# Kernel tuning notes

Hardware: AMD Instinct MI355X
Metric: run time of the kernel (lower is better)

## Reference

```python
import jax, jax.numpy as jnp
import numpy as np

B, L, H, HEADS = 4, 2048, 512, 8
D = H // HEADS  # 64


def setup_inputs() -> dict:
    key = jax.random.key(0)
    ks = jax.random.split(key, 13)
    s = 0.02
    return {
        "q_in": jax.random.normal(ks[0], (B, L, H), jnp.float32),
        "k_in": jax.random.normal(ks[1], (B, L, H), jnp.float32),
        "v_in": jax.random.normal(ks[2], (B, L, H), jnp.float32),
        "Wq_w": jax.random.normal(ks[3], (H, H), jnp.float32) * s,
        "Wq_b": jax.random.normal(ks[4], (H,), jnp.float32) * s,
        "Wk_w": jax.random.normal(ks[5], (H, H), jnp.float32) * s,
        "Wk_b": jax.random.normal(ks[6], (H,), jnp.float32) * s,
        "Wv_w": jax.random.normal(ks[7], (H, H), jnp.float32) * s,
        "Wv_b": jax.random.normal(ks[8], (H,), jnp.float32) * s,
        "Wo_w": jax.random.normal(ks[9], (H, H), jnp.float32) * s,
        "Wo_b": jax.random.normal(ks[10], (H,), jnp.float32) * s,
        "Wp_w": jax.random.normal(ks[11], (2 * L - 1, D), jnp.float32) * s,
        "Wp_b": jax.random.normal(ks[12], (2 * L - 1,), jnp.float32) * s,
    }


def _skew(p):
    # p: (b, h, l, 2l-1) -> relative-position bias (b, h, l, l) via pad/flatten/reshape skew trick
    b, h, l, _ = p.shape
    p = jnp.pad(p, ((0, 0), (0, 0), (0, 0), (0, 1)))          # (b,h,l,2l)
    p = p.reshape(b, h, 2 * l * l)
    p = jnp.pad(p, ((0, 0), (0, 0), (0, l - 1)))               # (b,h,(l+1)(2l-1))
    p = p.reshape(b, h, l + 1, 2 * l - 1)
    return p[:, :, :-1, -l:]                                   # (b,h,l,l)


def reference(q_in, k_in, v_in, Wq_w, Wq_b, Wk_w, Wk_b, Wv_w, Wv_b, Wo_w, Wo_b, Wp_w, Wp_b):
    b, l, hid = q_in.shape
    q = q_in @ Wq_w.T + Wq_b
    k = k_in @ Wk_w.T + Wk_b
    v = v_in @ Wv_w.T + Wv_b
    # (b, l, h*d) -> (b, h, l, d)
    to_heads = lambda x: x.reshape(b, l, HEADS, D).transpose(0, 2, 1, 3)
    q, k, v = to_heads(q), to_heads(k), to_heads(v)
    q = q / jnp.sqrt(jnp.asarray(D, q.dtype))  # scaling applied BEFORE posenc, as in original
    scores = jnp.einsum('bhid,bhjd->bhij', q, k)
    pos = _skew(q @ Wp_w.T + Wp_b)             # posenc linear applied to scaled q
    scores = scores + pos
    attn = jax.nn.softmax(scores, axis=-1)     # (b,h,l,l)
    # Original torch.einsum('b h l l, b h l d -> b h l d') takes the DIAGONAL of attn
    diag = jnp.diagonal(attn, axis1=-2, axis2=-1)  # (b,h,l)
    out = diag[..., None] * v                       # (b,h,l,d)
    out = out.transpose(0, 2, 1, 3).reshape(b, l, hid)
    return out @ Wo_w.T + Wo_b
```

## Files before the change

### kernel.cpp

```cpp
#include <hip/hip_runtime.h>
#include <cstdint>


typedef unsigned short u16;
typedef __bf16 bf16x8 __attribute__((ext_vector_type(8)));
typedef __bf16 bf16x2 __attribute__((ext_vector_type(2)));
typedef float  f32x16 __attribute__((ext_vector_type(16)));
typedef uint32_t __attribute__((address_space(1))) as1_u32;
typedef uint32_t __attribute__((address_space(3))) as3_u32;

__device__ __forceinline__ u16 f2bf(float f) {
  __bf16 h = (__bf16)f;
  return __builtin_bit_cast(u16, h);
}
__device__ __forceinline__ uint32_t pkbf(float a, float b) {
  bf16x2 v; v[0] = (__bf16)a; v[1] = (__bf16)b;
  return __builtin_bit_cast(uint32_t, v);
}
__device__ __forceinline__ float bf2f(u16 u) {
  return __uint_as_float(((uint32_t)u) << 16);
}
__device__ __forceinline__ void gl_lds16(const void* g, void* l) {
  __builtin_amdgcn_global_load_lds((const as1_u32*)g, (as3_u32*)l, 16, 0, 0);
}

__global__ __launch_bounds__(256) void prep_kernel(
    const float* __restrict__ qin, const float* __restrict__ kin, const float* __restrict__ vin,
    const float* __restrict__ wq,  const float* __restrict__ wk,  const float* __restrict__ wv,
    const float* __restrict__ wo,  const float* __restrict__ wp,
    u16* __restrict__ xq, u16* __restrict__ xk, u16* __restrict__ xv,
    u16* __restrict__ bwq, u16* __restrict__ bwk, u16* __restrict__ bwv,
    u16* __restrict__ bwo, u16* __restrict__ bwp) {
  long u = (long)blockIdx.x * 256 + threadIdx.x;
  const float* src; u16* dst; long off; float qs = 1.0f;
  if      (u < 524288L)  { src = qin; dst = xq;  off = u; }
  else if (u < 1048576L) { src = kin; dst = xk;  off = u - 524288L; }
  else if (u < 1572864L) { src = vin; dst = xv;  off = u - 1048576L; }
  else if (u < 1605632L) { src = wq;  dst = bwq; off = u - 1572864L; qs = 0.18033688f; }
  else if (u < 1638400L) { src = wk;  dst = bwk; off = u - 1605632L; }
  else if (u < 1671168L) { src = wv;  dst = bwv; off = u - 1638400L; }
  else if (u < 1703936L) { src = wo;  dst = bwo; off = u - 1671168L; }
  else if (u < 1736696L) { src = wp;  dst = bwp; off = u - 1703936L; }
  else {
    long o = (u - 1736696L) * 8 + 262080L;
    uint4 z = {0u, 0u, 0u, 0u};
    *(uint4*)(bwp + o) = z;
    return;
  }
  const float4* s4 = (const float4*)(src + off * 8);
  float4 a = s4[0], b = s4[1];
  uint32_t p0 = pkbf(a.x * qs, a.y * qs);
  uint32_t p1 = pkbf(a.z * qs, a.w * qs);
  uint32_t p2 = pkbf(b.x * qs, b.y * qs);
  uint32_t p3 = pkbf(b.z * qs, b.w * qs);
  uint4 o = {p0, p1, p2, p3};
  *(uint4*)(dst + off * 8) = o;
}

__global__ __launch_bounds__(256) void gemm_bt(
    const u16* __restrict__ A, const u16* __restrict__ W, const float* __restrict__ bias,
    float* __restrict__ ofp) {
  __shared__ u16 Al[128 * 32];
  __shared__ u16 Bl[128 * 32];
  const int tid = threadIdx.x;
  const int lane = tid & 63, w = tid >> 6;
  const int wi = w >> 1, wj = w & 1;
  const int m0 = (blockIdx.x >> 2) * 128, n0 = (blockIdx.x & 3) * 128;
  const int l31 = lane & 31;

  float bv0 = bias[n0 + 64 * wj + l31];
  float bv1 = bias[n0 + 64 * wj + 32 + l31];
  f32x16 acc[2][2];
#pragma unroll
  for (int i = 0; i < 2; ++i)
#pragma unroll
    for (int r = 0; r < 16; ++r) { acc[i][0][r] = bv0; acc[i][1][r] = bv1; }

  for (int kb = 0; kb < 16; ++kb) {
#pragma unroll
    for (int c = 0; c < 2; ++c) {
      int s = c * 256 + w * 64 + lane;
      int r = s >> 2, ch = s & 3;
      int gch = ch ^ ((r >> 1) & 3);
      gl_lds16(A + (long)(m0 + r) * 512 + kb * 32 + gch * 8, (char*)Al + (c * 256 + w * 64) * 16);
      gl_lds16(W + (long)(n0 + r) * 512 + kb * 32 + gch * 8, (char*)Bl + (c * 256 + w * 64) * 16);
    }
    __syncthreads();
    bf16x8 af[2][2], bfr[2][2];
#pragma unroll
    for (int mt = 0; mt < 2; ++mt)
#pragma unroll
      for (int ks = 0; ks < 2; ++ks) {
        int r = 64 * wi + 32 * mt + l31;
        int ch = 2 * ks + (lane >> 5);
        af[mt][ks] = *(const bf16x8*)((char*)Al + (r * 4 + (ch ^ ((r >> 1) & 3))) * 16);
      }
#pragma unroll
    for (int nt = 0; nt < 2; ++nt)
#pragma unroll
      for (int ks = 0; ks < 2; ++ks) {
        int r = 64 * wj + 32 * nt + l31;
        int ch = 2 * ks + (lane >> 5);
        bfr[nt][ks] = *(const bf16x8*)((char*)Bl + (r * 4 + (ch ^ ((r >> 1) & 3))) * 16);
      }
#pragma unroll
    for (int mt = 0; mt < 2; ++mt)
#pragma unroll
      for (int nt = 0; nt < 2; ++nt)
#pragma unroll
        for (int ks = 0; ks < 2; ++ks)
          acc[mt][nt] = __builtin_amdgcn_mfma_f32_32x32x16_bf16(af[mt][ks], bfr[nt][ks],
                                                                acc[mt][nt], 0, 0, 0);
    __syncthreads();
  }
#pragma unroll
  for (int nt = 0; nt < 2; ++nt) {
    int n = n0 + 64 * wj + 32 * nt + l31;
#pragma unroll
    for (int mt = 0; mt < 2; ++mt) {
#pragma unroll
      for (int r = 0; r < 16; ++r) {
        int row = m0 + 64 * wi + 32 * mt + (r & 3) + 8 * (r >> 2) + 4 * (lane >> 5);
        ofp[(long)row * 512 + n] = acc[mt][nt][r];
      }
    }
  }
}

__global__ __launch_bounds__(256) void qkv_gemm(
    const u16* __restrict__ xq, const u16* __restrict__ xk, const u16* __restrict__ xv,
    const u16* __restrict__ wqp, const u16* __restrict__ wkp, const u16* __restrict__ wvp,
    const float* __restrict__ bq, const float* __restrict__ bk, const float* __restrict__ bv,
    u16* __restrict__ oq, u16* __restrict__ ok, u16* __restrict__ ov) {
  __shared__ u16 Al[128 * 32];
  __shared__ u16 Bl[128 * 32];
  const int mat = blockIdx.x >> 8;
  const int tile = blockIdx.x & 255;
  const u16* A = (mat == 0) ? xq : (mat == 1) ? xk : xv;
  const u16* W = (mat == 0) ? wqp : (mat == 1) ? wkp : wvp;
  const float* bias = (mat == 0) ? bq : (mat == 1) ? bk : bv;
  u16* obf = (mat == 0) ? oq : (mat == 1) ? ok : ov;
  const float bsc = (mat == 0) ? 0.18033688f : 1.0f;

  const int tid = threadIdx.x;
  const int lane = tid & 63, w = tid >> 6;
  const int wi = w >> 1, wj = w & 1;
  const int m0 = (tile >> 2) * 128, n0 = (tile & 3) * 128;
  const int l31 = lane & 31;

  float bv0 = bias[n0 + 64 * wj + l31] * bsc;
  float bv1 = bias[n0 + 64 * wj + 32 + l31] * bsc;
  f32x16 acc[2][2];
#pragma unroll
  for (int i = 0; i < 2; ++i)
#pragma unroll
    for (int r = 0; r < 16; ++r) { acc[i][0][r] = bv0; acc[i][1][r] = bv1; }

  for (int kb = 0; kb < 16; ++kb) {
#pragma unroll
    for (int c = 0; c < 2; ++c) {
      int s = c * 256 + w * 64 + lane;
      int r = s >> 2, ch = s & 3;
      int gch = ch ^ ((r >> 1) & 3);
      gl_lds16(A + (long)(m0 + r) * 512 + kb * 32 + gch * 8, (char*)Al + (c * 256 + w * 64) * 16);
      gl_lds16(W + (long)(n0 + r) * 512 + kb * 32 + gch * 8, (char*)Bl + (c * 256 + w * 64) * 16);
    }
    __syncthreads();
    bf16x8 af[2][2], bfr[2][2];
#pragma unroll
    for (int mt = 0; mt < 2; ++mt)
#pragma unroll
      for (int ks = 0; ks < 2; ++ks) {
        int r = 64 * wi + 32 * mt + l31;
        int ch = 2 * ks + (lane >> 5);
        af[mt][ks] = *(const bf16x8*)((char*)Al + (r * 4 + (ch ^ ((r >> 1) & 3))) * 16);
      }
#pragma unroll
    for (int nt = 0; nt < 2; ++nt)
#pragma unroll
      for (int ks = 0; ks < 2; ++ks) {
        int r = 64 * wj + 32 * nt + l31;
        int ch = 2 * ks + (lane >> 5);
        bfr[nt][ks] = *(const bf16x8*)((char*)Bl + (r * 4 + (ch ^ ((r >> 1) & 3))) * 16);
      }
#pragma unroll
    for (int mt = 0; mt < 2; ++mt)
#pragma unroll
      for (int nt = 0; nt < 2; ++nt)
#pragma unroll
        for (int ks = 0; ks < 2; ++ks)
          acc[mt][nt] = __builtin_amdgcn_mfma_f32_32x32x16_bf16(af[mt][ks], bfr[nt][ks],
                                                                acc[mt][nt], 0, 0, 0);
    __syncthreads();
  }
#pragma unroll
  for (int nt = 0; nt < 2; ++nt) {
    int n = n0 + 64 * wj + 32 * nt + l31;
#pragma unroll
    for (int mt = 0; mt < 2; ++mt) {
#pragma unroll
      for (int r = 0; r < 16; ++r) {
        int row = m0 + 64 * wi + 32 * mt + (r & 3) + 8 * (r >> 2) + 4 * (lane >> 5);
        int b = row >> 11, l = row & 2047, h = n >> 6, d = n & 63;
        obf[(((long)(b * 8 + h)) * 2048 + l) * 64 + d] = f2bf(acc[mt][nt][r]);
      }
    }
  }
}

__global__ __launch_bounds__(256, 4) void attn_kernel(
    const u16* __restrict__ qw, const u16* __restrict__ kw, const u16* __restrict__ vw,
    const u16* __restrict__ wpw, const float* __restrict__ wpb, u16* __restrict__ outp) {
  __shared__ u16 Pl[283 * 66];
  __shared__ float sdiag[64];
  __shared__ float rssum[128];
  __shared__ float attw[64];

  const int tid = threadIdx.x, lane = tid & 63, w = tid >> 6;
  const int wi = w >> 1, wj = w & 1;
  const int sbi = blockIdx.x;
  const int kk_ = sbi >> 3;
  const int bh = (sbi & 7) + 8 * (kk_ >> 5);
  const int it = kk_ & 31;
  const int i0 = it * 64, base = 1984 - i0;
  const u16* qb = qw + (long)bh * 2048 * 64;
  const u16* kb = kw + (long)bh * 2048 * 64;
  const u16* vb = vw + (long)bh * 2048 * 64;

  const int l31 = lane & 31, lh = lane >> 5;
  const int iibase = 32 * wi + 4 * lh;

  bf16x8 aq[4];
  {
    int row = i0 + 32 * wi + l31;
    const u16* p = qb + (long)row * 64 + lh * 8;
#pragma unroll
    for (int kk = 0; kk < 4; ++kk) aq[kk] = *(const bf16x8*)(p + kk * 16);
  }

  float rsum[16];
#pragma unroll
  for (int r = 0; r < 16; ++r) rsum[r] = 0.f;

  auto pblock = [&](int g) {
    int brow = base + 64 * g + 32 * wj + l31;
    const u16* bp = wpw + (long)brow * 64 + lh * 8;
    int bidx = brow > 4094 ? 4094 : brow;
    float bv = wpb[bidx] * 1.44269504f;
    f32x16 accP;
#pragma unroll
    for (int r = 0; r < 16; ++r) accP[r] = bv;
#pragma unroll
    for (int kk = 0; kk < 4; ++kk) {
      bf16x8 bw = *(const bf16x8*)(bp + kk * 16);
      accP = __builtin_amdgcn_mfma_f32_32x32x16_bf16(aq[kk], bw, accP, 0, 0, 0);
    }
    int colp = (g & 3) * 64 + 32 * wj + l31;
    uint32_t pk0[8];
#pragma unroll
    for (int m = 0; m < 4; ++m) {
      pk0[2 * m]     = pkbf(accP[4 * m + 0], accP[4 * m + 1]);
      pk0[2 * m + 1] = pkbf(accP[4 * m + 2], accP[4 * m + 3]);
    }
    u16* wl = &Pl[colp * 66 + iibase];
#pragma unroll
    for (int m = 0; m < 4; ++m) {
      *(uint32_t*)(wl + 8 * m) = pk0[2 * m];
      *(uint32_t*)(wl + 8 * m + 2) = pk0[2 * m + 1];
    }
    if (((g & 3) == 0) && (wj == 0)) {
      if (l31 < 27) {
        u16* wl2 = wl + 256 * 66;
#pragma unroll
        for (int m = 0; m < 4; ++m) {
          *(uint32_t*)(wl2 + 8 * m) = pk0[2 * m];
          *(uint32_t*)(wl2 + 8 * m + 2) = pk0[2 * m + 1];
        }
      }
    }
  };

  pblock(0);
  pblock(1);

  const int W1c = 63 + 32 * wj + l31 - iibase;

  for (int jt = 0; jt < 32; ++jt) {
    bf16x8 kf[4];
    {
      const u16* bp = kb + (long)(jt * 64 + 32 * wj + l31) * 64 + lh * 8;
#pragma unroll
      for (int kk = 0; kk < 4; ++kk) kf[kk] = *(const bf16x8*)(bp + kk * 16);
    }
    if (jt <= 30) pblock(jt + 2);
    __syncthreads();

    f32x16 accS;
    {
      int W1 = 64 * jt + W1c;
      int b_ = ((W1 - 27) & 255) + 27;
      const u16* rb = &Pl[b_ * 66 + iibase - 27 * 65];
#pragma unroll
      for (int r = 0; r < 16; ++r) {
        const int lrr = (r & 3) + 8 * (r >> 2);
        accS[r] = bf2f(rb[(27 - lrr) * 65]);
      }
    }
#pragma unroll
    for (int kk = 0; kk < 4; ++kk)
      accS = __builtin_amdgcn_mfma_f32_32x32x16_bf16(aq[kk], kf[kk], accS, 0, 0, 0);
#pragma unroll
    for (int r = 0; r < 16; ++r) rsum[r] += exp2f(accS[r]);

    if ((jt == it) && (wi == wj)) {
#pragma unroll
      for (int r = 0; r < 16; ++r) {
        const int lrr = (r & 3) + 8 * (r >> 2);
        if ((lrr + 4 * lh) == l31) sdiag[32 * wi + l31] = accS[r];
      }
    }
  }

#pragma unroll
  for (int r = 0; r < 16; ++r) {
    float v = rsum[r];
    v += __shfl_xor(v, 1);
    v += __shfl_xor(v, 2);
    v += __shfl_xor(v, 4);
    v += __shfl_xor(v, 8);
    v += __shfl_xor(v, 16);
    rsum[r] = v;
  }
  if (l31 == 0) {
#pragma unroll
    for (int r = 0; r < 16; ++r) {
      int lr = (r & 3) + 8 * (r >> 2) + 4 * lh;
      rssum[(32 * wi + lr) * 2 + wj] = rsum[r];
    }
  }
  __syncthreads();
  if (tid < 64) {
    float S = rssum[2 * tid] + rssum[2 * tid + 1];
    attw[tid] = exp2f(sdiag[tid]) / S;
  }
  __syncthreads();
  {
    int r = tid >> 2, dd = (tid & 3) * 16;
    float a = attw[r];
    int b = bh >> 3, h = bh & 7;
    const u16* vp = vb + (long)(i0 + r) * 64 + dd;
    u16* op = outp + ((long)(b * 2048 + i0 + r)) * 512 + h * 64 + dd;
    uint4 v0 = *(const uint4*)vp;
    uint4 v1 = *(const uint4*)(vp + 8);
    uint32_t vin[8] = {v0.x, v0.y, v0.z, v0.w, v1.x, v1.y, v1.z, v1.w};
    uint32_t vout[8];
#pragma unroll
    for (int e = 0; e < 8; ++e) {
      float lo = bf2f((u16)(vin[e] & 0xffffu)) * a;
      float hi = bf2f((u16)(vin[e] >> 16)) * a;
      vout[e] = pkbf(lo, hi);
    }
    uint4 o0 = {vout[0], vout[1], vout[2], vout[3]};
    uint4 o1 = {vout[4], vout[5], vout[6], vout[7]};
    *(uint4*)op = o0;
    *(uint4*)(op + 8) = o1;
  }
}

extern "C" void kernel_launch(void* const* d_in, const int* in_sizes, int n_in,
                              void* d_out, int out_size, void* d_ws, size_t ws_size,
                              hipStream_t stream) {
  (void)in_sizes; (void)n_in; (void)out_size; (void)ws_size;
  const float* q_in = (const float*)d_in[0];
  const float* k_in = (const float*)d_in[1];
  const float* v_in = (const float*)d_in[2];
  const float* Wq_w = (const float*)d_in[3];
  const float* Wq_b = (const float*)d_in[4];
  const float* Wk_w = (const float*)d_in[5];
  const float* Wk_b = (const float*)d_in[6];
  const float* Wv_w = (const float*)d_in[7];
  const float* Wv_b = (const float*)d_in[8];
  const float* Wo_w = (const float*)d_in[9];
  const float* Wo_b = (const float*)d_in[10];
  const float* Wp_w = (const float*)d_in[11];
  const float* Wp_b = (const float*)d_in[12];

  char* ws = (char*)d_ws;
  u16* xq   = (u16*)(ws + 0);
  u16* xk   = (u16*)(ws + 8388608);
  u16* xv   = (u16*)(ws + 16777216);
  u16* wq   = (u16*)(ws + 25165824);
  u16* wk   = (u16*)(ws + 25690112);
  u16* wv   = (u16*)(ws + 26214400);
  u16* wo   = (u16*)(ws + 26738688);
  u16* wp   = (u16*)(ws + 27262976);
  u16* q_ws = (u16*)(ws + 27787264);
  u16* k_ws = (u16*)(ws + 36175872);
  u16* v_ws = (u16*)(ws + 44564480);
  u16* opre = (u16*)(ws + 52953088);

  prep_kernel<<<6784, 256, 0, stream>>>(q_in, k_in, v_in, Wq_w, Wk_w, Wv_w, Wo_w, Wp_w,
                                        xq, xk, xv, wq, wk, wv, wo, wp);
  qkv_gemm<<<768, 256, 0, stream>>>(xq, xk, xv, wq, wk, wv, Wq_b, Wk_b, Wv_b,
                                    q_ws, k_ws, v_ws);
  attn_kernel<<<1024, 256, 0, stream>>>(q_ws, k_ws, v_ws, wp, Wp_b, opre);
  gemm_bt<<<256, 256, 0, stream>>>(opre, wo, Wo_b, (float*)d_out);
}
```

Measured before the change: 273.0 us.

## Shrink GEMM tiles to 64x64, prefetch attention bias and use raw v_exp

Both projection GEMMs move from 128x128 to 64x64 tiles with a swizzled block order, which quadruples the grid so more CUs are busy, at the cost of less operand reuse per block. In the attention kernel, the next block's positional bias and the next skewed bias values from LDS are loaded one iteration ahead, and the Wp fragment loads are issued before the MFMAs. exp2f is replaced with inline v_exp_f32, dropping the range handling exp2f adds. Launch bounds change: the attention kernel goes from 4 to 3 waves per SIMD and the GEMMs now request 4.

Measured after the change: 273.5 us. Within noise of the previous version (+0.2%).

```diff
diff --git a/kernel.cpp b/kernel.cpp
--- a/kernel.cpp
+++ b/kernel.cpp
@@ -19,6 +19,11 @@
 }
 __device__ __forceinline__ float bf2f(u16 u) {
   return __uint_as_float(((uint32_t)u) << 16);
+}
+__device__ __forceinline__ float exp2v(float x) {
+  float r;
+  asm("v_exp_f32 %0, %1" : "=v"(r) : "v"(x));
+  return r;
 }
 __device__ __forceinline__ void gl_lds16(const void* g, void* l) {
   __builtin_amdgcn_global_load_lds((const as1_u32*)g, (as3_u32*)l, 16, 0, 0);
@@ -57,85 +62,70 @@
   *(uint4*)(dst + off * 8) = o;
 }
 
-__global__ __launch_bounds__(256) void gemm_bt(
+__device__ __forceinline__ void gemm64_core(
+    const u16* __restrict__ A, const u16* __restrict__ W, int m0, int n0,
+    u16* Al, u16* Bl, int tid, f32x16& acc) {
+  const int lane = tid & 63, w = tid >> 6;
+  const int wi = w >> 1, wj = w & 1;
+  const int l31 = lane & 31, lh = lane >> 5;
+  const int r = tid >> 2, ch = tid & 3;
+  const int gch = ch ^ ((r >> 1) & 3);
+  for (int kb = 0; kb < 16; ++kb) {
+    gl_lds16(A + (long)(m0 + r) * 512 + kb * 32 + gch * 8, (char*)Al + w * 64 * 16);
+    gl_lds16(W + (long)(n0 + r) * 512 + kb * 32 + gch * 8, (char*)Bl + w * 64 * 16);
+    __syncthreads();
+    bf16x8 af[2], bfr[2];
+#pragma unroll
+    for (int ks = 0; ks < 2; ++ks) {
+      int c2 = 2 * ks + lh;
+      int rA = 32 * wi + l31;
+      int rB = 32 * wj + l31;
+      af[ks]  = *(const bf16x8*)((char*)Al + (rA * 4 + (c2 ^ ((rA >> 1) & 3))) * 16);
+      bfr[ks] = *(const bf16x8*)((char*)Bl + (rB * 4 + (c2 ^ ((rB >> 1) & 3))) * 16);
+    }
+#pragma unroll
+    for (int ks = 0; ks < 2; ++ks)
+      acc = __builtin_amdgcn_mfma_f32_32x32x16_bf16(af[ks], bfr[ks], acc, 0, 0, 0);
+    __syncthreads();
+  }
+}
+
+__global__ __launch_bounds__(256, 4) void gemm_bt(
     const u16* __restrict__ A, const u16* __restrict__ W, const float* __restrict__ bias,
     float* __restrict__ ofp) {
-  __shared__ u16 Al[128 * 32];
-  __shared__ u16 Bl[128 * 32];
+  __shared__ u16 Al[64 * 32];
+  __shared__ u16 Bl[64 * 32];
   const int tid = threadIdx.x;
   const int lane = tid & 63, w = tid >> 6;
   const int wi = w >> 1, wj = w & 1;
-  const int m0 = (blockIdx.x >> 2) * 128, n0 = (blockIdx.x & 3) * 128;
-  const int l31 = lane & 31;
-
-  float bv0 = bias[n0 + 64 * wj + l31];
-  float bv1 = bias[n0 + 64 * wj + 32 + l31];
-  f32x16 acc[2][2];
-#pragma unroll
-  for (int i = 0; i < 2; ++i)
-#pragma unroll
-    for (int r = 0; r < 16; ++r) { acc[i][0][r] = bv0; acc[i][1][r] = bv1; }
-
-  for (int kb = 0; kb < 16; ++kb) {
-#pragma unroll
-    for (int c = 0; c < 2; ++c) {
-      int s = c * 256 + w * 64 + lane;
-      int r = s >> 2, ch = s & 3;
-      int gch = ch ^ ((r >> 1) & 3);
-      gl_lds16(A + (long)(m0 + r) * 512 + kb * 32 + gch * 8, (char*)Al + (c * 256 + w * 64) * 16);
-      gl_lds16(W + (long)(n0 + r) * 512 + kb * 32 + gch * 8, (char*)Bl + (c * 256 + w * 64) * 16);
-    }
-    __syncthreads();
-    bf16x8 af[2][2], bfr[2][2];
-#pragma unroll
-    for (int mt = 0; mt < 2; ++mt)
-#pragma unroll
-      for (int ks = 0; ks < 2; ++ks) {
-        int r = 64 * wi + 32 * mt + l31;
-        int ch = 2 * ks + (lane >> 5);
-        af[mt][ks] = *(const bf16x8*)((char*)Al + (r * 4 + (ch ^ ((r >> 1) & 3))) * 16);
-      }
-#pragma unroll
-    for (int nt = 0; nt < 2; ++nt)
-#pragma unroll
-      for (int ks = 0; ks < 2; ++ks) {
-        int r = 64 * wj + 32 * nt + l31;
-        int ch = 2 * ks + (lane >> 5);
-        bfr[nt][ks] = *(const bf16x8*)((char*)Bl + (r * 4 + (ch ^ ((r >> 1) & 3))) * 16);
-      }
-#pragma unroll
-    for (int mt = 0; mt < 2; ++mt)
-#pragma unroll
-      for (int nt = 0; nt < 2; ++nt)
-#pragma unroll
-        for (int ks = 0; ks < 2; ++ks)
-          acc[mt][nt] = __builtin_amdgcn_mfma_f32_32x32x16_bf16(af[mt][ks], bfr[nt][ks],
-                                                                acc[mt][nt], 0, 0, 0);
-    __syncthreads();
-  }
-#pragma unroll
-  for (int nt = 0; nt < 2; ++nt) {
-    int n = n0 + 64 * wj + 32 * nt + l31;
-#pragma unroll
-    for (int mt = 0; mt < 2; ++mt) {
-#pragma unroll
-      for (int r = 0; r < 16; ++r) {
-        int row = m0 + 64 * wi + 32 * mt + (r & 3) + 8 * (r >> 2) + 4 * (lane >> 5);
-        ofp[(long)row * 512 + n] = acc[mt][nt][r];
-      }
-    }
-  }
-}
-
-__global__ __launch_bounds__(256) void qkv_gemm(
+  const int l31 = lane & 31, lh = lane >> 5;
+  const int u = (blockIdx.x & 7) * 128 + (blockIdx.x >> 3);
+  const int m0 = (u >> 3) * 64, n0 = (u & 7) * 64;
+
+  float bv = bias[n0 + 32 * wj + l31];
+  f32x16 acc;
+#pragma unroll
+  for (int rr = 0; rr < 16; ++rr) acc[rr] = bv;
+
+  gemm64_core(A, W, m0, n0, Al, Bl, tid, acc);
+
+  int n = n0 + 32 * wj + l31;
+#pragma unroll
+  for (int rr = 0; rr < 16; ++rr) {
+    int row = m0 + 32 * wi + (rr & 3) + 8 * (rr >> 2) + 4 * lh;
+    ofp[(long)row * 512 + n] = acc[rr];
+  }
+}
+
+__global__ __launch_bounds__(256, 4) void qkv_gemm(
     const u16* __restrict__ xq, const u16* __restrict__ xk, const u16* __restrict__ xv,
     const u16* __restrict__ wqp, const u16* __restrict__ wkp, const u16* __restrict__ wvp,
     const float* __restrict__ bq, const float* __restrict__ bk, const float* __restrict__ bv,
     u16* __restrict__ oq, u16* __restrict__ ok, u16* __restrict__ ov) {
-  __shared__ u16 Al[128 * 32];
-  __shared__ u16 Bl[128 * 32];
-  const int mat = blockIdx.x >> 8;
-  const int tile = blockIdx.x & 255;
+  __shared__ u16 Al[64 * 32];
+  __shared__ u16 Bl[64 * 32];
+  const int mat = blockIdx.x >> 10;
+  const int t = blockIdx.x & 1023;
   const u16* A = (mat == 0) ? xq : (mat == 1) ? xk : xv;
   const u16* W = (mat == 0) ? wqp : (mat == 1) ? wkp : wvp;
   const float* bias = (mat == 0) ? bq : (mat == 1) ? bk : bv;
@@ -145,70 +135,28 @@
   const int tid = threadIdx.x;
   const int lane = tid & 63, w = tid >> 6;
   const int wi = w >> 1, wj = w & 1;
-  const int m0 = (tile >> 2) * 128, n0 = (tile & 3) * 128;
-  const int l31 = lane & 31;
-
-  float bv0 = bias[n0 + 64 * wj + l31] * bsc;
-  float bv1 = bias[n0 + 64 * wj + 32 + l31] * bsc;
-  f32x16 acc[2][2];
-#pragma unroll
-  for (int i = 0; i < 2; ++i)
-#pragma unroll
-    for (int r = 0; r < 16; ++r) { acc[i][0][r] = bv0; acc[i][1][r] = bv1; }
-
-  for (int kb = 0; kb < 16; ++kb) {
-#pragma unroll
-    for (int c = 0; c < 2; ++c) {
-      int s = c * 256 + w * 64 + lane;
-      int r = s >> 2, ch = s & 3;
-      int gch = ch ^ ((r >> 1) & 3);
-      gl_lds16(A + (long)(m0 + r) * 512 + kb * 32 + gch * 8, (char*)Al + (c * 256 + w * 64) * 16);
-      gl_lds16(W + (long)(n0 + r) * 512 + kb * 32 + gch * 8, (char*)Bl + (c * 256 + w * 64) * 16);
-    }
-    __syncthreads();
-    bf16x8 af[2][2], bfr[2][2];
-#pragma unroll
-    for (int mt = 0; mt < 2; ++mt)
-#pragma unroll
-      for (int ks = 0; ks < 2; ++ks) {
-        int r = 64 * wi + 32 * mt + l31;
-        int ch = 2 * ks + (lane >> 5);
-        af[mt][ks] = *(const bf16x8*)((char*)Al + (r * 4 + (ch ^ ((r >> 1) & 3))) * 16);
-      }
-#pragma unroll
-    for (int nt = 0; nt < 2; ++nt)
-#pragma unroll
-      for (int ks = 0; ks < 2; ++ks) {
-        int r = 64 * wj + 32 * nt + l31;
-        int ch = 2 * ks + (lane >> 5);
-        bfr[nt][ks] = *(const bf16x8*)((char*)Bl + (r * 4 + (ch ^ ((r >> 1) & 3))) * 16);
-      }
-#pragma unroll
-    for (int mt = 0; mt < 2; ++mt)
-#pragma unroll
-      for (int nt = 0; nt < 2; ++nt)
-#pragma unroll
-        for (int ks = 0; ks < 2; ++ks)
-          acc[mt][nt] = __builtin_amdgcn_mfma_f32_32x32x16_bf16(af[mt][ks], bfr[nt][ks],
-                                                                acc[mt][nt], 0, 0, 0);
-    __syncthreads();
-  }
-#pragma unroll
-  for (int nt = 0; nt < 2; ++nt) {
-    int n = n0 + 64 * wj + 32 * nt + l31;
-#pragma unroll
-    for (int mt = 0; mt < 2; ++mt) {
-#pragma unroll
-      for (int r = 0; r < 16; ++r) {
-        int row = m0 + 64 * wi + 32 * mt + (r & 3) + 8 * (r >> 2) + 4 * (lane >> 5);
-        int b = row >> 11, l = row & 2047, h = n >> 6, d = n & 63;
-        obf[(((long)(b * 8 + h)) * 2048 + l) * 64 + d] = f2bf(acc[mt][nt][r]);
-      }
-    }
-  }
-}
-
-__global__ __launch_bounds__(256, 4) void attn_kernel(
+  const int l31 = lane & 31, lh = lane >> 5;
+  const int u = (t & 7) * 128 + (t >> 3);
+  const int m0 = (u >> 3) * 64, n0 = (u & 7) * 64;
+
+  float bvv = bias[n0 + 32 * wj + l31] * bsc;
+  f32x16 acc;
+#pragma unroll
+  for (int rr = 0; rr < 16; ++rr) acc[rr] = bvv;
+
+  gemm64_core(A, W, m0, n0, Al, Bl, tid, acc);
+
+  int n = n0 + 32 * wj + l31;
+  int h = n >> 6, d = n & 63;
+#pragma unroll
+  for (int rr = 0; rr < 16; ++rr) {
+    int row = m0 + 32 * wi + (rr & 3) + 8 * (rr >> 2) + 4 * lh;
+    int b = row >> 11, l = row & 2047;
+    obf[(((long)(b * 8 + h)) * 2048 + l) * 64 + d] = f2bf(acc[rr]);
+  }
+}
+
+__global__ __launch_bounds__(256, 3) void attn_kernel(
     const u16* __restrict__ qw, const u16* __restrict__ kw, const u16* __restrict__ vw,
     const u16* __restrict__ wpw, const float* __restrict__ wpb, u16* __restrict__ outp) {
   __shared__ u16 Pl[283 * 66];
@@ -242,19 +190,25 @@
 #pragma unroll
   for (int r = 0; r < 16; ++r) rsum[r] = 0.f;
 
-  auto pblock = [&](int g) {
-    int brow = base + 64 * g + 32 * wj + l31;
-    const u16* bp = wpw + (long)brow * 64 + lh * 8;
+  const int browc = base + 32 * wj + l31;
+
+  auto ldbias = [&](int g) -> float {
+    int brow = browc + 64 * g;
     int bidx = brow > 4094 ? 4094 : brow;
-    float bv = wpb[bidx] * 1.44269504f;
+    return wpb[bidx] * 1.44269504f;
+  };
+
+  auto pblock = [&](int g, float bv) {
+    const u16* bp = wpw + (long)(browc + 64 * g) * 64 + lh * 8;
+    bf16x8 bw[4];
+#pragma unroll
+    for (int kk = 0; kk < 4; ++kk) bw[kk] = *(const bf16x8*)(bp + kk * 16);
     f32x16 accP;
 #pragma unroll
     for (int r = 0; r < 16; ++r) accP[r] = bv;
 #pragma unroll
-    for (int kk = 0; kk < 4; ++kk) {
-      bf16x8 bw = *(const bf16x8*)(bp + kk * 16);
-      accP = __builtin_amdgcn_mfma_f32_32x32x16_bf16(aq[kk], bw, accP, 0, 0, 0);
-    }
+    for (int kk = 0; kk < 4; ++kk)
+      accP = __builtin_amdgcn_mfma_f32_32x32x16_bf16(aq[kk], bw[kk], accP, 0, 0, 0);
     int colp = (g & 3) * 64 + 32 * wj + l31;
     uint32_t pk0[8];
 #pragma unroll
@@ -268,22 +222,32 @@
       *(uint32_t*)(wl + 8 * m) = pk0[2 * m];
       *(uint32_t*)(wl + 8 * m + 2) = pk0[2 * m + 1];
     }
-    if (((g & 3) == 0) && (wj == 0)) {
-      if (l31 < 27) {
-        u16* wl2 = wl + 256 * 66;
-#pragma unroll
-        for (int m = 0; m < 4; ++m) {
-          *(uint32_t*)(wl2 + 8 * m) = pk0[2 * m];
-          *(uint32_t*)(wl2 + 8 * m + 2) = pk0[2 * m + 1];
-        }
+    if (((g & 3) == 0) && (wj == 0) && (l31 < 27)) {
+      u16* wl2 = wl + 256 * 66;
+#pragma unroll
+      for (int m = 0; m < 4; ++m) {
+        *(uint32_t*)(wl2 + 8 * m) = pk0[2 * m];
+        *(uint32_t*)(wl2 + 8 * m + 2) = pk0[2 * m + 1];
       }
     }
   };
 
-  pblock(0);
-  pblock(1);
+  pblock(0, ldbias(0));
+  pblock(1, ldbias(1));
+  float bvc = ldbias(2);
+  __syncthreads();
 
   const int W1c = 63 + 32 * wj + l31 - iibase;
+  uint32_t pc[16];
+  {
+    int b_ = ((W1c - 27) & 255) + 27;
+    const u16* rb = &Pl[b_ * 66 + iibase - 27 * 65];
+#pragma unroll
+    for (int r = 0; r < 16; ++r) {
+      const int lrr = (r & 3) + 8 * (r >> 2);
+      pc[r] = rb[(27 - lrr) * 65];
+    }
+  }
 
   for (int jt = 0; jt < 32; ++jt) {
     bf16x8 kf[4];
@@ -292,25 +256,30 @@
 #pragma unroll
       for (int kk = 0; kk < 4; ++kk) kf[kk] = *(const bf16x8*)(bp + kk * 16);
     }
-    if (jt <= 30) pblock(jt + 2);
+    float bvn = (jt <= 29) ? ldbias(jt + 3) : 0.f;
+    if (jt <= 30) pblock(jt + 2, bvc);
     __syncthreads();
 
-    f32x16 accS;
-    {
-      int W1 = 64 * jt + W1c;
+    uint32_t pn[16];
+    if (jt <= 30) {
+      int W1 = 64 * (jt + 1) + W1c;
       int b_ = ((W1 - 27) & 255) + 27;
       const u16* rb = &Pl[b_ * 66 + iibase - 27 * 65];
 #pragma unroll
       for (int r = 0; r < 16; ++r) {
         const int lrr = (r & 3) + 8 * (r >> 2);
-        accS[r] = bf2f(rb[(27 - lrr) * 65]);
+        pn[r] = rb[(27 - lrr) * 65];
       }
     }
+
+    f32x16 accS;
+#pragma unroll
+    for (int r = 0; r < 16; ++r) accS[r] = __uint_as_float(pc[r] << 16);
 #pragma unroll
     for (int kk = 0; kk < 4; ++kk)
       accS = __builtin_amdgcn_mfma_f32_32x32x16_bf16(aq[kk], kf[kk], accS, 0, 0, 0);
 #pragma unroll
-    for (int r = 0; r < 16; ++r) rsum[r] += exp2f(accS[r]);
+    for (int r = 0; r < 16; ++r) rsum[r] += exp2v(accS[r]);
 
     if ((jt == it) && (wi == wj)) {
 #pragma unroll
@@ -319,6 +288,9 @@
         if ((lrr + 4 * lh) == l31) sdiag[32 * wi + l31] = accS[r];
       }
     }
+#pragma unroll
+    for (int r = 0; r < 16; ++r) pc[r] = pn[r];
+    bvc = bvn;
   }
 
 #pragma unroll
@@ -341,7 +313,7 @@
   __syncthreads();
   if (tid < 64) {
     float S = rssum[2 * tid] + rssum[2 * tid + 1];
-    attw[tid] = exp2f(sdiag[tid]) / S;
+    attw[tid] = exp2v(sdiag[tid]) / S;
   }
   __syncthreads();
   {
@@ -401,8 +373,8 @@
 
   prep_kernel<<<6784, 256, 0, stream>>>(q_in, k_in, v_in, Wq_w, Wk_w, Wv_w, Wo_w, Wp_w,
                                         xq, xk, xv, wq, wk, wv, wo, wp);
-  qkv_gemm<<<768, 256, 0, stream>>>(xq, xk, xv, wq, wk, wv, Wq_b, Wk_b, Wv_b,
-                                    q_ws, k_ws, v_ws);
+  qkv_gemm<<<3072, 256, 0, stream>>>(xq, xk, xv, wq, wk, wv, Wq_b, Wk_b, Wv_b,
+                                     q_ws, k_ws, v_ws);
   attn_kernel<<<1024, 256, 0, stream>>>(q_ws, k_ws, v_ws, wp, Wp_b, opre);
-  gemm_bt<<<256, 256, 0, stream>>>(opre, wo, Wo_b, (float*)d_out);
-}
+  gemm_bt<<<1024, 256, 0, stream>>>(opre, wo, Wo_b, (float*)d_out);
+}
```
